# Performance work log

Hardware: AMD Instinct MI355X
Metric: run time of the kernel (lower is better)

The kernel has to match this reference:

```python
import jax, jax.numpy as jnp
import numpy as np

# physics constants (match init_kwargs)
DT = 1.0 / 60.0
G_ACC = 9.81
RHO = 1.225
CD = 0.47
NU = 0.001
B, N, GRID = 512, 64, 16


def _norm(x):
    return jnp.linalg.norm(x, axis=-1, keepdims=True)


def _deriv(pos, vel, rot, omega, mass, inertia, contacts, fluid_v,
           Fext, tau, log_A, log_k, log_b, conv_w):
    g_vec = jnp.array([0.0, 0.0, -G_ACC], dtype=pos.dtype)
    Fg = mass[..., None] * g_vec                                  # [B,N,3]
    A = jax.nn.softplus(log_A).reshape(1, -1, 1)
    vm = jnp.maximum(_norm(vel), 1e-6)
    Fd = -0.5 * RHO * CD * A * vm * vel                           # drag
    k = jax.nn.softplus(log_k)
    b = jax.nn.softplus(log_b)
    d_ij = pos[:, None, :, :] - pos[:, :, None, :]                # [B,N,N,3] = p_j - p_i
    dist = jnp.maximum(_norm(d_ij), 1e-6)
    n_hat = d_ij / dist
    pen = jax.nn.relu(1.0 - dist[..., 0])                         # penetration depth
    dvel = vel[:, None, :, :] - vel[:, :, None, :]                # v_j - v_i
    Fc = (k * pen[..., None] * n_hat + b * dvel * contacts[..., None]).sum(axis=2)
    dv = (Fext + Fg + Fd + Fc) / mass[..., None]
    Io = inertia * omega
    domega = (tau - jnp.cross(omega, Io)) / jnp.maximum(inertia, 1e-6)
    w, x, y, z = rot[..., 0], rot[..., 1], rot[..., 2], rot[..., 3]
    ox, oy, oz = omega[..., 0], omega[..., 1], omega[..., 2]
    drot = 0.5 * jnp.stack([
        -x * ox - y * oy - z * oz,
        w * ox + y * oz - z * oy,
        w * oy - x * oz + z * ox,
        w * oz + x * oy - y * ox], axis=-1)
    P_in = (Fext * vel).sum((-1, -2))
    P_dis = -(Fd * vel).sum((-1, -2))
    dE = P_in - P_dis
    Bsz = fluid_v.shape[0]
    u = fluid_v.reshape(Bsz, GRID, GRID, GRID, 3).transpose(0, 4, 1, 2, 3)  # NCDHW
    dfluid = NU * jax.lax.conv_general_dilated(
        u, conv_w, window_strides=(1, 1, 1), padding=[(1, 1)] * 3,
        feature_group_count=3,
        dimension_numbers=('NCDHW', 'OIDHW', 'NCDHW'))
    dfluid = dfluid.transpose(0, 2, 3, 4, 1).reshape(Bsz, GRID ** 3, 3)
    return vel, dv, drot, domega, dE, dfluid


def _quat_normalize(q):
    return q / jnp.maximum(_norm(q), 1e-12)


def _apply(pos, vel, rot, omega, fluid_v, dt, dp, dv, dr, dw, dfluid):
    npos = pos + dt * dp
    nvel = vel + dt * dv
    nrot = _quat_normalize(rot + dt * dr)
    nomega = omega + dt * dw
    new_u = fluid_v + dt * dfluid
    nfluid = new_u - new_u.mean(axis=1, keepdims=True)
    return npos, nvel, nrot, nomega, nfluid


def _forward(pos, vel, rot, omega, mass, inertia, contacts, energy, fluid_v,
             Fext, tau, log_A, log_k, log_b, conv_w):
    dt = DT
    params = (mass, inertia, contacts)

    def deriv(p, v, r, o, fv):
        return _deriv(p, v, r, o, mass, inertia, contacts, fv,
                      Fext, tau, log_A, log_k, log_b, conv_w)

    k1 = deriv(pos, vel, rot, omega, fluid_v)
    s2 = _apply(pos, vel, rot, omega, fluid_v, dt / 2, k1[0], k1[1], k1[2], k1[3], k1[5])
    k2 = deriv(*s2)
    s3 = _apply(pos, vel, rot, omega, fluid_v, dt / 2, k2[0], k2[1], k2[2], k2[3], k2[5])
    k3 = deriv(*s3)
    s4 = _apply(pos, vel, rot, omega, fluid_v, dt, k3[0], k3[1], k3[2], k3[3], k3[5])
    k4 = deriv(*s4)

    def rk4c(y, a, b_, c, d):
        return y + dt / 6 * (a + 2 * b_ + 2 * c + d)

    npos = rk4c(pos, k1[0], k2[0], k3[0], k4[0])
    nvel = rk4c(vel, k1[1], k2[1], k3[1], k4[1])
    nrot = _quat_normalize(rk4c(rot, k1[2], k2[2], k3[2], k4[2]))
    nomega = rk4c(omega, k1[3], k2[3], k3[3], k4[3])
    nenergy = rk4c(energy, k1[4], k2[4], k3[4], k4[4])
    nforces = Fext + mass[..., None] * k1[1]
    raw_fluid = rk4c(fluid_v, k1[5], k2[5], k3[5], k4[5])
    nfluid = raw_fluid - raw_fluid.mean(axis=1, keepdims=True)
    Bsz = pos.shape[0]
    # flatten new state: [pos, vel, rot, omega, forces, energy, fluid_v]
    return jnp.concatenate([
        npos.reshape(Bsz, -1), nvel.reshape(Bsz, -1), nrot.reshape(Bsz, -1),
        nomega.reshape(Bsz, -1), nforces.reshape(Bsz, -1),
        nenergy[:, None], nfluid.reshape(Bsz, -1)], axis=-1)


def setup_inputs() -> dict:
    key = jax.random.key(0)
    ks = jax.random.split(key, 12)
    rot = jax.random.normal(ks[2], (B, N, 4), dtype=jnp.float32)
    rot = rot / jnp.maximum(jnp.linalg.norm(rot, axis=-1, keepdims=True), 1e-12)
    return {
        'pos': 2.0 * jax.random.normal(ks[0], (B, N, 3), dtype=jnp.float32),
        'vel': jax.random.normal(ks[1], (B, N, 3), dtype=jnp.float32),
        'rot': rot,
        'omega': jax.random.normal(ks[3], (B, N, 3), dtype=jnp.float32),
        'mass': 0.5 + jax.random.uniform(ks[4], (B, N), dtype=jnp.float32),
        'inertia': 0.05 + 0.1 * jax.random.uniform(ks[5], (B, N, 3), dtype=jnp.float32),
        'contacts': jax.random.uniform(ks[6], (B, N, N), dtype=jnp.float32),
        'energy': jnp.zeros((B,), dtype=jnp.float32),
        'fluid_v': jax.random.normal(ks[7], (B, GRID ** 3, 3), dtype=jnp.float32),
        'Fext': jax.random.normal(ks[8], (B, N, 3), dtype=jnp.float32),
        'tau': jax.random.normal(ks[9], (B, N, 3), dtype=jnp.float32),
        'log_A': jnp.zeros((N,), dtype=jnp.float32),
        'log_k': jnp.full((1,), np.log(1000.0), dtype=jnp.float32),
        'log_b': jnp.full((1,), np.log(10.0), dtype=jnp.float32),
        'conv_w': 0.1 * jax.random.normal(ks[10], (3, 1, 3, 3, 3), dtype=jnp.float32),
    }


def reference(pos, vel, rot, omega, mass, inertia, contacts, energy, fluid_v,
              Fext, tau, log_A, log_k, log_b, conv_w):
    return _forward(pos, vel, rot, omega, mass, inertia, contacts, energy,
                    fluid_v, Fext, tau, log_A, log_k, log_b, conv_w)
```

## Files before the change

kernel.cpp:

```cpp
#include <hip/hip_runtime.h>

#define DT (1.0f/60.0f)
#define G_ACC 9.81f
#define RHO 1.225f
#define CD_ 0.47f
#define NU 0.001f

__device__ __forceinline__ float softplus_f(float x) {
    return log1pf(expf(-fabsf(x))) + fmaxf(x, 0.0f);
}

#define RL(v, l) __int_as_float(__builtin_amdgcn_readlane(__float_as_int(v), (l)))

__device__ __forceinline__ float dpp_xm(float v) {
    return __int_as_float(__builtin_amdgcn_update_dpp(0, __float_as_int(v), 0x111, 0xf, 0xf, true));
}
__device__ __forceinline__ float dpp_xp(float v) {
    return __int_as_float(__builtin_amdgcn_update_dpp(0, __float_as_int(v), 0x101, 0xf, 0xf, true));
}

__global__ __launch_bounds__(256) void particle_kernel(
    const float* __restrict__ pos, const float* __restrict__ vel,
    const float* __restrict__ rot, const float* __restrict__ omega,
    const float* __restrict__ mass, const float* __restrict__ inertia,
    const float* __restrict__ contacts, const float* __restrict__ energy,
    const float* __restrict__ Fext, const float* __restrict__ tau,
    const float* __restrict__ log_A, const float* __restrict__ log_k,
    const float* __restrict__ log_b, float* __restrict__ out)
{
    const int b = blockIdx.x;
    const int t = threadIdx.x;
    const int q = t >> 6;
    const int i = t & 63;

    __shared__ float sF[2][4][192];

    const float* cbase = contacts + (size_t)b*4096 + (size_t)i*64 + q*16;
    float4 cA = ((const float4*)cbase)[0];
    float4 cB = ((const float4*)cbase)[1];
    float4 cC = ((const float4*)cbase)[2];
    float4 cD = ((const float4*)cbase)[3];
    float cj[16] = {cA.x,cA.y,cA.z,cA.w, cB.x,cB.y,cB.z,cB.w,
                    cC.x,cC.y,cC.z,cC.w, cD.x,cD.y,cD.z,cD.w};

    const size_t p3 = ((size_t)b*64 + i)*3;
    const size_t p4 = ((size_t)b*64 + i)*4;
    float bpx=pos[p3],   bpy=pos[p3+1],   bpz=pos[p3+2];
    float bvx=vel[p3],   bvy=vel[p3+1],   bvz=vel[p3+2];
    float brw=rot[p4],   brx=rot[p4+1],   bry=rot[p4+2],  brz=rot[p4+3];
    float box=omega[p3], boy=omega[p3+1], boz=omega[p3+2];
    float m  = mass[(size_t)b*64+i];
    float Ix=inertia[p3], Iy=inertia[p3+1], Iz=inertia[p3+2];
    float Fex=Fext[p3],   Fey=Fext[p3+1],   Fez=Fext[p3+2];
    float tx=tau[p3],     ty=tau[p3+1],     tz=tau[p3+2];
    float Ai = softplus_f(log_A[i]);
    float kc = softplus_f(log_k[0]);
    float bc = softplus_f(log_b[0]);
    float dragc = -0.5f * RHO * CD_ * Ai;
    float invm  = 1.0f / m;
    float iIx = 1.0f/fmaxf(Ix,1e-6f), iIy = 1.0f/fmaxf(Iy,1e-6f), iIz = 1.0f/fmaxf(Iz,1e-6f);

    float cpx=bpx, cpy=bpy, cpz=bpz;
    float cvx=bvx, cvy=bvy, cvz=bvz;
    float crw=brw, crx=brx, cry=bry, crz=brz;
    float cox=box, coy=boy, coz=boz;

    float apx=0,apy=0,apz=0, avx=0,avy=0,avz=0;
    float arw=0,arx=0,ary=0,arz=0, awx=0,awy=0,awz=0;
    float eacc=0.f;
    float k1vx=0,k1vy=0,k1vz=0;

    const float wgt[4] = {1.f, 2.f, 2.f, 1.f};
    const float hs[4]  = {DT*0.5f, DT*0.5f, DT, 0.f};
    const int j0 = q << 4;

    for (int s = 0; s < 4; ++s) {
        float Fcx=0.f, Fcy=0.f, Fcz=0.f;
        #pragma unroll
        for (int jj = 0; jj < 16; ++jj) {
            const int j = j0 + jj;
            float pjx = RL(cpx, j), pjy = RL(cpy, j), pjz = RL(cpz, j);
            float vjx = RL(cvx, j), vjy = RL(cvy, j), vjz = RL(cvz, j);
            float dx = pjx - cpx, dy = pjy - cpy, dz = pjz - cpz;
            float d2 = dx*dx + dy*dy + dz*dz;
            float dist = fmaxf(sqrtf(d2), 1e-6f);
            float pen  = fmaxf(1.0f - dist, 0.0f);
            float coef = kc * pen * __builtin_amdgcn_rcpf(dist);
            float cbj  = bc * cj[jj];
            Fcx += coef*dx + cbj*(vjx - cvx);
            Fcy += coef*dy + cbj*(vjy - cvy);
            Fcz += coef*dz + cbj*(vjz - cvz);
        }
        const int buf = s & 1;
        sF[buf][q][i*3+0] = Fcx;
        sF[buf][q][i*3+1] = Fcy;
        sF[buf][q][i*3+2] = Fcz;
        __syncthreads();
        Fcx = sF[buf][0][i*3+0] + sF[buf][1][i*3+0] + sF[buf][2][i*3+0] + sF[buf][3][i*3+0];
        Fcy = sF[buf][0][i*3+1] + sF[buf][1][i*3+1] + sF[buf][2][i*3+1] + sF[buf][3][i*3+1];
        Fcz = sF[buf][0][i*3+2] + sF[buf][1][i*3+2] + sF[buf][2][i*3+2] + sF[buf][3][i*3+2];

        float vm = fmaxf(sqrtf(cvx*cvx+cvy*cvy+cvz*cvz), 1e-6f);
        float dc = dragc * vm;
        float Fdx = dc*cvx, Fdy = dc*cvy, Fdz = dc*cvz;

        float dvx = (Fex + Fdx + Fcx) * invm;
        float dvy = (Fey + Fdy + Fcy) * invm;
        float dvz = (Fez - m*G_ACC + Fdz + Fcz) * invm;

        float dqw = 0.5f*(-crx*cox - cry*coy - crz*coz);
        float dqx = 0.5f*( crw*cox + cry*coz - crz*coy);
        float dqy = 0.5f*( crw*coy - crx*coz + crz*cox);
        float dqz = 0.5f*( crw*coz + crx*coy - cry*cox);

        float Iox = Ix*cox, Ioy = Iy*coy, Ioz = Iz*coz;
        float cxv = coy*Ioz - coz*Ioy;
        float cyv = coz*Iox - cox*Ioz;
        float czv = cox*Ioy - coy*Iox;
        float dwx = (tx - cxv) * iIx;
        float dwy = (ty - cyv) * iIy;
        float dwz = (tz - czv) * iIz;

        float ei = (Fex+Fdx)*cvx + (Fey+Fdy)*cvy + (Fez+Fdz)*cvz;
        #pragma unroll
        for (int off = 32; off > 0; off >>= 1) ei += __shfl_xor(ei, off, 64);

        float w = wgt[s];
        eacc += w * ei;
        if (s == 0) { k1vx=dvx; k1vy=dvy; k1vz=dvz; }
        apx += w*cvx; apy += w*cvy; apz += w*cvz;
        avx += w*dvx; avy += w*dvy; avz += w*dvz;
        arw += w*dqw; arx += w*dqx; ary += w*dqy; arz += w*dqz;
        awx += w*dwx; awy += w*dwy; awz += w*dwz;

        if (s < 3) {
            float h = hs[s];
            float npx = bpx + h*cvx, npy = bpy + h*cvy, npz = bpz + h*cvz;
            cvx = bvx + h*dvx; cvy = bvy + h*dvy; cvz = bvz + h*dvz;
            cpx = npx; cpy = npy; cpz = npz;
            float qw = brw + h*dqw, qx = brx + h*dqx, qy = bry + h*dqy, qz = brz + h*dqz;
            float iqn = 1.0f / fmaxf(sqrtf(qw*qw+qx*qx+qy*qy+qz*qz), 1e-12f);
            crw = qw*iqn; crx = qx*iqn; cry = qy*iqn; crz = qz*iqn;
            cox = box + h*dwx; coy = boy + h*dwy; coz = boz + h*dwz;
        }
    }

    if (q == 0) {
        const float s6 = DT / 6.0f;
        float* ob = out + (size_t)b * 13313;
        ob[      i*3+0] = bpx + s6*apx;  ob[      i*3+1] = bpy + s6*apy;  ob[      i*3+2] = bpz + s6*apz;
        ob[192 + i*3+0] = bvx + s6*avx;  ob[192 + i*3+1] = bvy + s6*avy;  ob[192 + i*3+2] = bvz + s6*avz;
        {
            float qw=brw+s6*arw, qx=brx+s6*arx, qy=bry+s6*ary, qz=brz+s6*arz;
            float iq = 1.0f / fmaxf(sqrtf(qw*qw+qx*qx+qy*qy+qz*qz), 1e-12f);
            ob[384 + i*4+0]=qw*iq; ob[384 + i*4+1]=qx*iq; ob[384 + i*4+2]=qy*iq; ob[384 + i*4+3]=qz*iq;
        }
        ob[640 + i*3+0] = box + s6*awx;  ob[640 + i*3+1] = boy + s6*awy;  ob[640 + i*3+2] = boz + s6*awz;
        ob[832 + i*3+0] = Fex + m*k1vx;  ob[832 + i*3+1] = Fey + m*k1vy;  ob[832 + i*3+2] = Fez + m*k1vz;
        if (i == 0) ob[1024] = energy[b] + s6*eacc;
    }
}

#define CSTR 17
#define CHPL (256*CSTR)

__global__ __launch_bounds__(768) void fluid_kernel(
    const float* __restrict__ fluid, const float* __restrict__ conv_w,
    float* __restrict__ out)
{
    const int b   = blockIdx.x;
    const int t   = threadIdx.x;
    const int ch  = t >> 8;
    const int col = t & 255;
    const int y   = col >> 4;
    const int wv  = t >> 6;

    __shared__ float u[3*CHPL];
    __shared__ float wsh[81];
    __shared__ float red[12];

    if (t < 81) wsh[t] = conv_w[t];

    const int lb = ch*CHPL + col*CSTR;
    const float* fb = fluid + (size_t)b*12288 + 3*col + ch;

    float base[16], acc[16], f[16];
    #pragma unroll
    for (int z = 0; z < 16; ++z) {
        float v = fb[z*768];
        base[z] = v; f[z] = v; acc[z] = 0.f;
        u[lb + z] = v;
    }
    __syncthreads();

    const float* W = wsh + ch*27;
    const int   cm = (y > 0)  ? lb - 16*CSTR : lb;
    const int   cp = (y < 15) ? lb + 16*CSTR : lb;
    const float mmask = (y > 0)  ? 1.f : 0.f;
    const float pmask = (y < 15) ? 1.f : 0.f;

    const float wgt[4] = {1.f, 2.f, 2.f, 1.f};
    const float hs[3]  = {DT*0.5f, DT*0.5f, DT};
    float mean = 0.f;

    #define ACC3(c, wi) { \
        float w0_ = W[wi], w1_ = W[9+(wi)], w2_ = W[18+(wi)]; \
        _Pragma("unroll") for (int z = 0; z < 16; ++z) o[z] += w1_ * (c)[z]; \
        _Pragma("unroll") for (int z = 1; z < 16; ++z) o[z] += w0_ * (c)[z-1]; \
        _Pragma("unroll") for (int z = 0; z < 15; ++z) o[z] += w2_ * (c)[z+1]; }

    for (int s = 0; s < 4; ++s) {
        float o[16];
        #pragma unroll
        for (int z = 0; z < 16; ++z) o[z] = 0.f;

        {
            float cl[16], cr[16];
            #pragma unroll
            for (int z = 0; z < 16; ++z) { cl[z] = dpp_xm(f[z]); cr[z] = dpp_xp(f[z]); }
            ACC3(f,  4);
            ACC3(cl, 3);
            ACC3(cr, 5);
        }
        {
            float c0[16], cl[16], cr[16];
            #pragma unroll
            for (int z = 0; z < 16; ++z) c0[z] = (u[cm + z] - mean) * mmask;
            #pragma unroll
            for (int z = 0; z < 16; ++z) { cl[z] = dpp_xm(c0[z]); cr[z] = dpp_xp(c0[z]); }
            ACC3(c0, 1);
            ACC3(cl, 0);
            ACC3(cr, 2);
        }
        {
            float c0[16], cl[16], cr[16];
            #pragma unroll
            for (int z = 0; z < 16; ++z) c0[z] = (u[cp + z] - mean) * pmask;
            #pragma unroll
            for (int z = 0; z < 16; ++z) { cl[z] = dpp_xm(c0[z]); cr[z] = dpp_xp(c0[z]); }
            ACC3(c0, 7);
            ACC3(cl, 6);
            ACC3(cr, 8);
        }

        float w = wgt[s];
        if (s < 3) {
            float h = hs[s];
            __syncthreads();
            float ps = 0.f;
            #pragma unroll
            for (int z = 0; z < 16; ++z) {
                float k = NU * o[z];
                acc[z] += w * k;
                float v = base[z] + h * k;
                u[lb + z] = v;
                f[z] = v;
                ps += v;
            }
            #pragma unroll
            for (int off = 32; off > 0; off >>= 1) ps += __shfl_xor(ps, off, 64);
            if ((t & 63) == 0) red[wv] = ps;
            __syncthreads();
            mean = (red[(ch<<2)] + red[(ch<<2)+1] + red[(ch<<2)+2] + red[(ch<<2)+3]) * (1.0f/4096.0f);
            #pragma unroll
            for (int z = 0; z < 16; ++z) f[z] -= mean;
        } else {
            #pragma unroll
            for (int z = 0; z < 16; ++z) acc[z] += w * NU * o[z];
        }
    }

    float raw[16];
    float ps = 0.f;
    #pragma unroll
    for (int z = 0; z < 16; ++z) { raw[z] = base[z] + (DT/6.0f)*acc[z]; ps += raw[z]; }
    #pragma unroll
    for (int off = 32; off > 0; off >>= 1) ps += __shfl_xor(ps, off, 64);
    __syncthreads();
    if ((t & 63) == 0) red[wv] = ps;
    __syncthreads();
    mean = (red[(ch<<2)] + red[(ch<<2)+1] + red[(ch<<2)+2] + red[(ch<<2)+3]) * (1.0f/4096.0f);

    float* ob = out + (size_t)b*13313 + 1025 + 3*col + ch;
    #pragma unroll
    for (int z = 0; z < 16; ++z) ob[z*768] = raw[z] - mean;
}

extern "C" void kernel_launch(void* const* d_in, const int* in_sizes, int n_in,
                              void* d_out, int out_size, void* d_ws, size_t ws_size,
                              hipStream_t stream) {
    const float* pos      = (const float*)d_in[0];
    const float* vel      = (const float*)d_in[1];
    const float* rot      = (const float*)d_in[2];
    const float* omega    = (const float*)d_in[3];
    const float* mass     = (const float*)d_in[4];
    const float* inertia  = (const float*)d_in[5];
    const float* contacts = (const float*)d_in[6];
    const float* energy   = (const float*)d_in[7];
    const float* fluid_v  = (const float*)d_in[8];
    const float* Fext     = (const float*)d_in[9];
    const float* tau      = (const float*)d_in[10];
    const float* log_A    = (const float*)d_in[11];
    const float* log_k    = (const float*)d_in[12];
    const float* log_b    = (const float*)d_in[13];
    const float* conv_w   = (const float*)d_in[14];
    float* out = (float*)d_out;

    particle_kernel<<<dim3(512), dim3(256), 0, stream>>>(
        pos, vel, rot, omega, mass, inertia, contacts, energy,
        Fext, tau, log_A, log_k, log_b, out);
    fluid_kernel<<<dim3(512), dim3(768), 0, stream>>>(fluid_v, conv_w, out);
}
```

Measured before the change: 167.0 us.

## Fuse particle and fluid kernels into one launch with per-channel fluid blocks

Merges the particle and fluid kernels into a single launch of 2048 blocks of 256 threads. The first 1536 blocks each handle one fluid channel of one batch element, and the remaining blocks run the particle dynamics. The fluid path no longer subtracts the mean from neighbor values before convolving. Instead it applies the mean correction algebraically through precomputed boundary-aware weight sums, and it reduces the mean per channel within one block. This removes a kernel launch, lets the two workloads overlap, and shrinks fluid blocks from 768 to 256 threads with less shared memory, which should improve occupancy. The cost is a per-element mean-times-weight-sum term, whose boundary handling must exactly match the masked stencil.

```diff
diff --git a/kernel.cpp b/kernel.cpp
--- a/kernel.cpp
+++ b/kernel.cpp
@@ -19,21 +19,147 @@
     return __int_as_float(__builtin_amdgcn_update_dpp(0, __float_as_int(v), 0x101, 0xf, 0xf, true));
 }
 
-__global__ __launch_bounds__(256) void particle_kernel(
+__global__ __launch_bounds__(256) void fused_kernel(
     const float* __restrict__ pos, const float* __restrict__ vel,
     const float* __restrict__ rot, const float* __restrict__ omega,
     const float* __restrict__ mass, const float* __restrict__ inertia,
     const float* __restrict__ contacts, const float* __restrict__ energy,
-    const float* __restrict__ Fext, const float* __restrict__ tau,
-    const float* __restrict__ log_A, const float* __restrict__ log_k,
-    const float* __restrict__ log_b, float* __restrict__ out)
+    const float* __restrict__ fluid, const float* __restrict__ Fext,
+    const float* __restrict__ tau, const float* __restrict__ log_A,
+    const float* __restrict__ log_k, const float* __restrict__ log_b,
+    const float* __restrict__ conv_w, float* __restrict__ out)
 {
-    const int b = blockIdx.x;
+    __shared__ float smem[4384];
     const int t = threadIdx.x;
+
+    if (blockIdx.x < 1536) {
+        const int b  = blockIdx.x & 511;
+        const int ch = blockIdx.x >> 9;
+        const int x  = t & 15, y = t >> 4, wv = t >> 6;
+        float* u   = smem;
+        float* wch = smem + 4352;
+        float* red = smem + 4380;
+        if (t < 27) wch[t] = conv_w[ch*27 + t];
+
+        const int lb = t*17;
+        const float* fb = fluid + (size_t)b*12288 + 3*t + ch;
+        float base[16], acc[16];
+        #pragma unroll
+        for (int z = 0; z < 16; ++z) {
+            float v = fb[z*768];
+            base[z] = v; acc[z] = 0.f; u[lb + z] = v;
+        }
+        __syncthreads();
+
+        const float mm = (y > 0)  ? 1.f : 0.f;
+        const float pm = (y < 15) ? 1.f : 0.f;
+        const float xm = (x > 0)  ? 1.f : 0.f;
+        const float xp = (x < 15) ? 1.f : 0.f;
+        const int   cm = (y > 0)  ? lb - 272 : lb;
+        const int   cp = (y < 15) ? lb + 272 : lb;
+
+        float Sdz[3];
+        #pragma unroll
+        for (int dz = 0; dz < 3; ++dz) {
+            float a0 = wch[dz*9+0]*xm + wch[dz*9+1] + wch[dz*9+2]*xp;
+            float a1 = wch[dz*9+3]*xm + wch[dz*9+4] + wch[dz*9+5]*xp;
+            float a2 = wch[dz*9+6]*xm + wch[dz*9+7] + wch[dz*9+8]*xp;
+            Sdz[dz] = mm*a0 + a1 + pm*a2;
+        }
+        const float SzLo  = Sdz[1] + Sdz[2];
+        const float SzMid = Sdz[0] + Sdz[1] + Sdz[2];
+        const float SzHi  = Sdz[0] + Sdz[1];
+        const float* W = wch + 0;
+
+        const float wgt[4] = {1.f, 2.f, 2.f, 1.f};
+        const float hs[3]  = {DT*0.5f, DT*0.5f, DT};
+        float mean = 0.f;
+
+        #define ACC3(c, wi) { \
+            float w0_ = W[wi], w1_ = W[9+(wi)], w2_ = W[18+(wi)]; \
+            _Pragma("unroll") for (int z = 0; z < 16; ++z) o[z] += w1_ * (c)[z]; \
+            _Pragma("unroll") for (int z = 1; z < 16; ++z) o[z] += w0_ * (c)[z-1]; \
+            _Pragma("unroll") for (int z = 0; z < 15; ++z) o[z] += w2_ * (c)[z+1]; }
+
+        for (int s = 0; s < 4; ++s) {
+            float o[16];
+            #pragma unroll
+            for (int z = 0; z < 16; ++z) o[z] = 0.f;
+
+            {
+                float c0[16], cl[16], cr[16];
+                #pragma unroll
+                for (int z = 0; z < 16; ++z) c0[z] = u[lb + z];
+                #pragma unroll
+                for (int z = 0; z < 16; ++z) { cl[z] = dpp_xm(c0[z]); cr[z] = dpp_xp(c0[z]); }
+                ACC3(c0, 4); ACC3(cl, 3); ACC3(cr, 5);
+            }
+            {
+                float c0[16], cl[16], cr[16];
+                #pragma unroll
+                for (int z = 0; z < 16; ++z) c0[z] = u[cm + z] * mm;
+                #pragma unroll
+                for (int z = 0; z < 16; ++z) { cl[z] = dpp_xm(c0[z]); cr[z] = dpp_xp(c0[z]); }
+                ACC3(c0, 1); ACC3(cl, 0); ACC3(cr, 2);
+            }
+            {
+                float c0[16], cl[16], cr[16];
+                #pragma unroll
+                for (int z = 0; z < 16; ++z) c0[z] = u[cp + z] * pm;
+                #pragma unroll
+                for (int z = 0; z < 16; ++z) { cl[z] = dpp_xm(c0[z]); cr[z] = dpp_xp(c0[z]); }
+                ACC3(c0, 7); ACC3(cl, 6); ACC3(cr, 8);
+            }
+
+            float w = wgt[s];
+            if (s < 3) {
+                float h = hs[s], ps = 0.f, wn[16];
+                #pragma unroll
+                for (int z = 0; z < 16; ++z) {
+                    float Sz = (z == 0) ? SzLo : ((z == 15) ? SzHi : SzMid);
+                    float k = NU * (o[z] - mean * Sz);
+                    acc[z] += w * k;
+                    wn[z] = base[z] + h * k;
+                    ps += wn[z];
+                }
+                #pragma unroll
+                for (int off = 32; off > 0; off >>= 1) ps += __shfl_xor(ps, off, 64);
+                __syncthreads();
+                #pragma unroll
+                for (int z = 0; z < 16; ++z) u[lb + z] = wn[z];
+                if ((t & 63) == 0) red[wv] = ps;
+                __syncthreads();
+                mean = (red[0] + red[1] + red[2] + red[3]) * (1.0f/4096.0f);
+            } else {
+                #pragma unroll
+                for (int z = 0; z < 16; ++z) {
+                    float Sz = (z == 0) ? SzLo : ((z == 15) ? SzHi : SzMid);
+                    acc[z] += w * NU * (o[z] - mean * Sz);
+                }
+            }
+        }
+        #undef ACC3
+
+        float raw[16], ps = 0.f;
+        #pragma unroll
+        for (int z = 0; z < 16; ++z) { raw[z] = base[z] + (DT/6.0f)*acc[z]; ps += raw[z]; }
+        #pragma unroll
+        for (int off = 32; off > 0; off >>= 1) ps += __shfl_xor(ps, off, 64);
+        __syncthreads();
+        if ((t & 63) == 0) red[wv] = ps;
+        __syncthreads();
+        float mn = (red[0] + red[1] + red[2] + red[3]) * (1.0f/4096.0f);
+
+        float* ob = out + (size_t)b*13313 + 1025 + 3*t + ch;
+        #pragma unroll
+        for (int z = 0; z < 16; ++z) ob[z*768] = raw[z] - mn;
+        return;
+    }
+
+    const int b = blockIdx.x - 1536;
     const int q = t >> 6;
     const int i = t & 63;
-
-    __shared__ float sF[2][4][192];
+    #define SF(buf, qq, idx) smem[(buf)*768 + (qq)*192 + (idx)]
 
     const float* cbase = contacts + (size_t)b*4096 + (size_t)i*64 + q*16;
     float4 cA = ((const float4*)cbase)[0];
@@ -92,13 +218,13 @@
             Fcz += coef*dz + cbj*(vjz - cvz);
         }
         const int buf = s & 1;
-        sF[buf][q][i*3+0] = Fcx;
-        sF[buf][q][i*3+1] = Fcy;
-        sF[buf][q][i*3+2] = Fcz;
+        SF(buf, q, i*3+0) = Fcx;
+        SF(buf, q, i*3+1) = Fcy;
+        SF(buf, q, i*3+2) = Fcz;
         __syncthreads();
-        Fcx = sF[buf][0][i*3+0] + sF[buf][1][i*3+0] + sF[buf][2][i*3+0] + sF[buf][3][i*3+0];
-        Fcy = sF[buf][0][i*3+1] + sF[buf][1][i*3+1] + sF[buf][2][i*3+1] + sF[buf][3][i*3+1];
-        Fcz = sF[buf][0][i*3+2] + sF[buf][1][i*3+2] + sF[buf][2][i*3+2] + sF[buf][3][i*3+2];
+        Fcx = SF(buf,0,i*3+0) + SF(buf,1,i*3+0) + SF(buf,2,i*3+0) + SF(buf,3,i*3+0);
+        Fcy = SF(buf,0,i*3+1) + SF(buf,1,i*3+1) + SF(buf,2,i*3+1) + SF(buf,3,i*3+1);
+        Fcz = SF(buf,0,i*3+2) + SF(buf,1,i*3+2) + SF(buf,2,i*3+2) + SF(buf,3,i*3+2);
 
         float vm = fmaxf(sqrtf(cvx*cvx+cvy*cvy+cvz*cvz), 1e-6f);
         float dc = dragc * vm;
@@ -159,131 +285,7 @@
         ob[832 + i*3+0] = Fex + m*k1vx;  ob[832 + i*3+1] = Fey + m*k1vy;  ob[832 + i*3+2] = Fez + m*k1vz;
         if (i == 0) ob[1024] = energy[b] + s6*eacc;
     }
-}
-
-#define CSTR 17
-#define CHPL (256*CSTR)
-
-__global__ __launch_bounds__(768) void fluid_kernel(
-    const float* __restrict__ fluid, const float* __restrict__ conv_w,
-    float* __restrict__ out)
-{
-    const int b   = blockIdx.x;
-    const int t   = threadIdx.x;
-    const int ch  = t >> 8;
-    const int col = t & 255;
-    const int y   = col >> 4;
-    const int wv  = t >> 6;
-
-    __shared__ float u[3*CHPL];
-    __shared__ float wsh[81];
-    __shared__ float red[12];
-
-    if (t < 81) wsh[t] = conv_w[t];
-
-    const int lb = ch*CHPL + col*CSTR;
-    const float* fb = fluid + (size_t)b*12288 + 3*col + ch;
-
-    float base[16], acc[16], f[16];
-    #pragma unroll
-    for (int z = 0; z < 16; ++z) {
-        float v = fb[z*768];
-        base[z] = v; f[z] = v; acc[z] = 0.f;
-        u[lb + z] = v;
-    }
-    __syncthreads();
-
-    const float* W = wsh + ch*27;
-    const int   cm = (y > 0)  ? lb - 16*CSTR : lb;
-    const int   cp = (y < 15) ? lb + 16*CSTR : lb;
-    const float mmask = (y > 0)  ? 1.f : 0.f;
-    const float pmask = (y < 15) ? 1.f : 0.f;
-
-    const float wgt[4] = {1.f, 2.f, 2.f, 1.f};
-    const float hs[3]  = {DT*0.5f, DT*0.5f, DT};
-    float mean = 0.f;
-
-    #define ACC3(c, wi) { \
-        float w0_ = W[wi], w1_ = W[9+(wi)], w2_ = W[18+(wi)]; \
-        _Pragma("unroll") for (int z = 0; z < 16; ++z) o[z] += w1_ * (c)[z]; \
-        _Pragma("unroll") for (int z = 1; z < 16; ++z) o[z] += w0_ * (c)[z-1]; \
-        _Pragma("unroll") for (int z = 0; z < 15; ++z) o[z] += w2_ * (c)[z+1]; }
-
-    for (int s = 0; s < 4; ++s) {
-        float o[16];
-        #pragma unroll
-        for (int z = 0; z < 16; ++z) o[z] = 0.f;
-
-        {
-            float cl[16], cr[16];
-            #pragma unroll
-            for (int z = 0; z < 16; ++z) { cl[z] = dpp_xm(f[z]); cr[z] = dpp_xp(f[z]); }
-            ACC3(f,  4);
-            ACC3(cl, 3);
-            ACC3(cr, 5);
-        }
-        {
-            float c0[16], cl[16], cr[16];
-            #pragma unroll
-            for (int z = 0; z < 16; ++z) c0[z] = (u[cm + z] - mean) * mmask;
-            #pragma unroll
-            for (int z = 0; z < 16; ++z) { cl[z] = dpp_xm(c0[z]); cr[z] = dpp_xp(c0[z]); }
-            ACC3(c0, 1);
-            ACC3(cl, 0);
-            ACC3(cr, 2);
-        }
-        {
-            float c0[16], cl[16], cr[16];
-            #pragma unroll
-            for (int z = 0; z < 16; ++z) c0[z] = (u[cp + z] - mean) * pmask;
-            #pragma unroll
-            for (int z = 0; z < 16; ++z) { cl[z] = dpp_xm(c0[z]); cr[z] = dpp_xp(c0[z]); }
-            ACC3(c0, 7);
-            ACC3(cl, 6);
-            ACC3(cr, 8);
-        }
-
-        float w = wgt[s];
-        if (s < 3) {
-            float h = hs[s];
-            __syncthreads();
-            float ps = 0.f;
-            #pragma unroll
-            for (int z = 0; z < 16; ++z) {
-                float k = NU * o[z];
-                acc[z] += w * k;
-                float v = base[z] + h * k;
-                u[lb + z] = v;
-                f[z] = v;
-                ps += v;
-            }
-            #pragma unroll
-            for (int off = 32; off > 0; off >>= 1) ps += __shfl_xor(ps, off, 64);
-            if ((t & 63) == 0) red[wv] = ps;
-            __syncthreads();
-            mean = (red[(ch<<2)] + red[(ch<<2)+1] + red[(ch<<2)+2] + red[(ch<<2)+3]) * (1.0f/4096.0f);
-            #pragma unroll
-            for (int z = 0; z < 16; ++z) f[z] -= mean;
-        } else {
-            #pragma unroll
-            for (int z = 0; z < 16; ++z) acc[z] += w * NU * o[z];
-        }
-    }
-
-    float raw[16];
-    float ps = 0.f;
-    #pragma unroll
-    for (int z = 0; z < 16; ++z) { raw[z] = base[z] + (DT/6.0f)*acc[z]; ps += raw[z]; }
-    #pragma unroll
-    for (int off = 32; off > 0; off >>= 1) ps += __shfl_xor(ps, off, 64);
-    __syncthreads();
-    if ((t & 63) == 0) red[wv] = ps;
-    __syncthreads();
-    mean = (red[(ch<<2)] + red[(ch<<2)+1] + red[(ch<<2)+2] + red[(ch<<2)+3]) * (1.0f/4096.0f);
-
-    float* ob = out + (size_t)b*13313 + 1025 + 3*col + ch;
-    #pragma unroll
-    for (int z = 0; z < 16; ++z) ob[z*768] = raw[z] - mean;
+    #undef SF
 }
 
 extern "C" void kernel_launch(void* const* d_in, const int* in_sizes, int n_in,
@@ -306,8 +308,7 @@
     const float* conv_w   = (const float*)d_in[14];
     float* out = (float*)d_out;
 
-    particle_kernel<<<dim3(512), dim3(256), 0, stream>>>(
-        pos, vel, rot, omega, mass, inertia, contacts, energy,
-        Fext, tau, log_A, log_k, log_b, out);
-    fluid_kernel<<<dim3(512), dim3(768), 0, stream>>>(fluid_v, conv_w, out);
-}
+    fused_kernel<<<dim3(2048), dim3(256), 0, stream>>>(
+        pos, vel, rot, omega, mass, inertia, contacts, energy, fluid_v,
+        Fext, tau, log_A, log_k, log_b, conv_w, out);
+}
```

Result: faster. 158.7 us (-5.0%).
